# Optimization experiments

Measured on AMD Instinct MI355X. Metric: run time of the kernel, lower is better.

Reference implementation:

```python
import jax, jax.numpy as jnp
import numpy as np

B, T, D = 8, 2048, 1024   # batch, seq_len (== block_size), n_embed
HS = 128                   # head_size

def setup_inputs() -> dict:
    key = jax.random.key(0)
    kx, kk, kq, kv = jax.random.split(key, 4)
    s = D ** -0.5  # torch Linear default init scale ~ U(-1/sqrt(in), 1/sqrt(in))
    x  = jax.random.normal(kx, (B, T, D), dtype=jnp.float32)
    Wk = jax.random.uniform(kk, (HS, D), jnp.float32, -s, s)
    Wq = jax.random.uniform(kq, (HS, D), jnp.float32, -s, s)
    Wv = jax.random.uniform(kv, (HS, D), jnp.float32, -s, s)
    return {"x": x, "Wk": Wk, "Wq": Wq, "Wv": Wv}

def reference(x, Wk, Wq, Wv):
    # single-head causal self-attention; dropout disabled (eval mode)
    Tlen = x.shape[1]
    k = jnp.einsum('btd,hd->bth', x, Wk)   # [B,T,HS]
    q = jnp.einsum('btd,hd->bth', x, Wq)
    v = jnp.einsum('btd,hd->bth', x, Wv)
    scale = Wk.shape[0] ** -0.5
    scores = jnp.einsum('bth,bsh->bts', q, k) * scale   # [B,T,T]
    causal = jnp.tril(jnp.ones((Tlen, Tlen), dtype=bool))
    scores = jnp.where(causal, scores, -jnp.inf)
    weights = jax.nn.softmax(scores, axis=-1)
    out = jnp.einsum('bts,bsh->bth', weights, v)        # [B,T,HS]
    return out
```

## Files before the change

kernel.cpp:

```cpp
#include <hip/hip_runtime.h>
#include <hip/hip_bf16.h>
#include <math.h>

#define BATCH_N 8
#define SEQ_T   2048
#define DIM_D   1024
#define HS_N    128

using bf16x8_t = __attribute__((ext_vector_type(8))) __bf16;
using bf16x4_t = __attribute__((ext_vector_type(4))) __bf16;
using f32x4_t  = __attribute__((ext_vector_type(4))) float;

__device__ __forceinline__ f32x4_t mfma_16x16x32(bf16x8_t a, bf16x8_t b, f32x4_t c) {
  return __builtin_amdgcn_mfma_f32_16x16x32_bf16(a, b, c, 0, 0, 0);
}

__device__ __forceinline__ void async_cp16(const void* g, void* l) {
  __builtin_amdgcn_global_load_lds(
      (const __attribute__((address_space(1))) unsigned int*)g,
      (__attribute__((address_space(3))) unsigned int*)l, 16, 0, 0);
}

#define BAR()      __builtin_amdgcn_s_barrier()
#define FENCE()    asm volatile("" ::: "memory")
#define WAIT_VM(n) asm volatile("s_waitcnt vmcnt(" #n ")" ::: "memory")
#define WAIT_LGKM0 asm volatile("s_waitcnt lgkmcnt(0)" ::: "memory")

__global__ __launch_bounds__(256) void castw_kernel(
    const float* __restrict__ Wk, const float* __restrict__ Wq,
    const float* __restrict__ Wv, __bf16* __restrict__ Wb,
    unsigned int* __restrict__ km) {
  if (blockIdx.x == 0 && threadIdx.x < 8) km[threadIdx.x] = 0u;
  int idx = blockIdx.x * 256 + threadIdx.x;
  int e   = idx * 4;
  int row = e >> 10;
  int col = e & 1023;
  const float* src;
  float sc = 1.0f;
  if (row < 128) {
    src = Wk + row * DIM_D + col;
  } else if (row < 256) {
    src = Wq + (row - 128) * DIM_D + col;
    sc  = 0.08838834764831845f;
  } else {
    src = Wv + (row - 256) * DIM_D + col;
  }
  float4 v = *(const float4*)src;
  bf16x4_t o;
  o[0] = (__bf16)(v.x * sc); o[1] = (__bf16)(v.y * sc);
  o[2] = (__bf16)(v.z * sc); o[3] = (__bf16)(v.w * sc);
  *(bf16x4_t*)(Wb + e) = o;
}

__global__ __launch_bounds__(512, 2) void proj_kernel(
    const float* __restrict__ x, const __bf16* __restrict__ Wb,
    __bf16* __restrict__ Qb, __bf16* __restrict__ Kb, __bf16* __restrict__ Vt) {
  __shared__ __align__(16) char psmem[114688];
  __bf16* A = (__bf16*)psmem;

  const int tid  = threadIdx.x;
  const int lane = tid & 63;
  const int wave = tid >> 6;
  const int h    = wave >> 2;
  const int g    = wave & 3;
  const int lr = lane & 15;
  const int lq = lane >> 4;
  const int m0 = blockIdx.x * 64;

  f32x4_t acc[2][6];
  #pragma unroll
  for (int mt = 0; mt < 2; ++mt)
    #pragma unroll
    for (int nt = 0; nt < 6; ++nt) acc[mt][nt] = (f32x4_t){0.f, 0.f, 0.f, 0.f};

  auto stageB = [&](int bufi, int kt) {
    __bf16* Bs = (__bf16*)(psmem + 65536 + bufi * 24576);
    for (int c = wave; c < 24; c += 8) {
      const int row = c * 16 + (lane >> 2);
      const int u   = (lane & 3) ^ ((row >> 1) & 3);
      async_cp16(Wb + (size_t)row * DIM_D + kt * 32 + u * 8, Bs + c * 512);
    }
  };

  stageB(0, 0);

  for (int p = 0; p < 2; ++p) {
    __syncthreads();

    {
      const int r  = tid >> 3;
      const int t  = tid & 7;
      const float* xs = x + (size_t)(m0 + r) * DIM_D + p * 512;
      __bf16* as = A + r * 512;
      const int sw = r & 7;
      #pragma unroll
      for (int i = 0; i < 8; ++i) {
        const int u = t + 8 * i;
        float4 f0 = *(const float4*)(xs + u * 8);
        float4 f1 = *(const float4*)(xs + u * 8 + 4);
        bf16x8_t a;
        a[0] = (__bf16)f0.x; a[1] = (__bf16)f0.y;
        a[2] = (__bf16)f0.z; a[3] = (__bf16)f0.w;
        a[4] = (__bf16)f1.x; a[5] = (__bf16)f1.y;
        a[6] = (__bf16)f1.z; a[7] = (__bf16)f1.w;
        *(bf16x8_t*)(as + ((u ^ sw) * 8)) = a;
      }
    }
    __syncthreads();

    for (int kt2 = 0; kt2 < 16; ++kt2) {
      const int kt  = p * 16 + kt2;
      const int cur = kt & 1;
      if (kt + 1 < 32) {
        stageB(cur ^ 1, kt + 1);
        WAIT_VM(3);
      } else {
        WAIT_VM(0);
      }
      BAR();
      FENCE();
      const __bf16* Bs = (const __bf16*)(psmem + 65536 + cur * 24576);

      bf16x8_t af[2];
      #pragma unroll
      for (int mt = 0; mt < 2; ++mt) {
        const int ml = h * 32 + mt * 16 + lr;
        const int u  = kt2 * 4 + lq;
        af[mt] = *(const bf16x8_t*)(&A[ml * 512 + ((u ^ (ml & 7)) * 8)]);
      }
      bf16x8_t bfv[6];
      #pragma unroll
      for (int nt = 0; nt < 6; ++nt) {
        const int nl = g * 96 + nt * 16 + lr;
        bfv[nt] = *(const bf16x8_t*)(&Bs[nl * 32 + ((lq ^ ((nl >> 1) & 3)) * 8)]);
      }
      #pragma unroll
      for (int mt = 0; mt < 2; ++mt)
        #pragma unroll
        for (int nt = 0; nt < 6; ++nt)
          acc[mt][nt] = mfma_16x16x32(af[mt], bfv[nt], acc[mt][nt]);
      WAIT_LGKM0;
      BAR();
      FENCE();
    }
  }

  #pragma unroll
  for (int mt = 0; mt < 2; ++mt) {
    const int t0 = m0 + h * 32 + mt * 16 + lq * 4;
    #pragma unroll
    for (int nt = 0; nt < 6; ++nt) {
      const int nn = g * 96 + nt * 16 + lr;
      if (nn < 256) {
        __bf16* dst = (nn < 128) ? (Kb + nn) : (Qb + (nn - 128));
        #pragma unroll
        for (int r = 0; r < 4; ++r)
          dst[(size_t)(t0 + r) * HS_N] = (__bf16)acc[mt][nt][r];
      } else {
        const int bb = t0 >> 11;
        const int tl = t0 & 2047;
        bf16x4_t o;
        #pragma unroll
        for (int r = 0; r < 4; ++r) o[r] = (__bf16)acc[mt][nt][r];
        *(bf16x4_t*)(Vt + (size_t)bb * (HS_N * SEQ_T) + (size_t)(nn - 256) * SEQ_T + tl) = o;
      }
    }
  }
}

__global__ __launch_bounds__(256) void knorm_kernel(
    const __bf16* __restrict__ Kb, unsigned int* __restrict__ km) {
  const int t = blockIdx.x * 256 + threadIdx.x;
  const __bf16* kp = Kb + (size_t)t * HS_N;
  float ss = 0.f;
  #pragma unroll
  for (int i = 0; i < 16; ++i) {
    bf16x8_t v = *(const bf16x8_t*)(kp + i * 8);
    #pragma unroll
    for (int j = 0; j < 8; ++j) { float f = (float)v[j]; ss += f * f; }
  }
  #pragma unroll
  for (int off = 1; off < 64; off <<= 1) ss = fmaxf(ss, __shfl_xor(ss, off));
  if ((threadIdx.x & 63) == 0) atomicMax(km + (t >> 11), __float_as_uint(ss));
}

__global__ __launch_bounds__(256, 2) void attn_kernel(
    const __bf16* __restrict__ Qb, const __bf16* __restrict__ Kb,
    const __bf16* __restrict__ Vt, const unsigned int* __restrict__ km,
    __bf16* __restrict__ Opart, float* __restrict__ lpart) {
  __shared__ __align__(16) char smem[81920];
  __bf16* KsBase = (__bf16*)smem;
  __bf16* VsBase = (__bf16*)(smem + 32768);
  float*  Ofl    = (float*)smem;

  const int lane = threadIdx.x & 63;
  const int wave = threadIdx.x >> 6;
  const int lr = lane & 15;
  const int lq = lane >> 4;
  const int bid  = blockIdx.x;
  const int b    = bid & 7;
  const int rest = bid >> 3;
  const int jg   = 15 - (rest >> 2);
  const int p4   = rest & 3;
  const int Q0   = jg * 128;
  const int qa   = Q0 + wave * 32;
  const int ch   = 2 * (jg + 1);
  const int c0   = (p4 * ch) >> 2;
  const int c1   = ((p4 + 1) * ch) >> 2;

  const __bf16* Qbb = Qb + (size_t)b * (SEQ_T * HS_N);
  const __bf16* Kbb = Kb + (size_t)b * (SEQ_T * HS_N);
  const __bf16* Vbb = Vt + (size_t)b * (HS_N * SEQ_T);
  __bf16* pbA = (__bf16*)(smem + 65536 + wave * 4096);
  __bf16* pbB = (__bf16*)(smem + 65536 + wave * 4096 + 2048);

  bf16x8_t qf[2][4];
  #pragma unroll
  for (int t = 0; t < 2; ++t)
    #pragma unroll
    for (int ks = 0; ks < 4; ++ks)
      qf[t][ks] = *(const bf16x8_t*)(Qbb + (size_t)(qa + t * 16 + lr) * HS_N
                                     + ks * 32 + lq * 8);

  const float km2 = __uint_as_float(km[b]);
  float mrow[2][4];
  #pragma unroll
  for (int t = 0; t < 2; ++t) {
    float qn2 = 0.f;
    #pragma unroll
    for (int ks = 0; ks < 4; ++ks)
      #pragma unroll
      for (int j = 0; j < 8; ++j) { float f = (float)qf[t][ks][j]; qn2 += f * f; }
    qn2 += __shfl_xor(qn2, 16);
    qn2 += __shfl_xor(qn2, 32);
    #pragma unroll
    for (int r2 = 0; r2 < 4; ++r2)
      mrow[t][r2] = sqrtf(__shfl(qn2, lq * 4 + r2) * km2);
  }

  f32x4_t Oa[2][8];
  #pragma unroll
  for (int t = 0; t < 2; ++t)
    #pragma unroll
    for (int o = 0; o < 8; ++o) Oa[t][o] = (f32x4_t){0.f, 0.f, 0.f, 0.f};
  float lsum[2][4] = {{0.f,0.f,0.f,0.f},{0.f,0.f,0.f,0.f}};

  auto stage = [&](int bufi, int c) {
    const int kk = c * 64;
    __bf16* Ks = KsBase + bufi * 8192;
    for (int idx = wave; idx < 32; idx += 4) {
      if (idx < 16) {
        const int row = idx * 4 + (lane >> 4);
        const int u   = (lane & 15) ^ (row & 15);
        async_cp16(Kbb + (size_t)(kk + row) * HS_N + u * 8, Ks + idx * 512);
      } else {
        const int i2  = idx - 16;
        const int row = i2 * 8 + (lane >> 3);
        const int u   = (lane & 7) ^ (row & 7);
        async_cp16(Vbb + (size_t)row * SEQ_T + kk + u * 8, VsBase + bufi * 8192 + i2 * 512);
      }
    }
  };

  if (c0 < c1) stage(0, c0);
  __syncthreads();

  for (int c = c0; c < c1; ++c) {
    const int cur = (c - c0) & 1;
    if (c + 1 < c1) {
      stage(cur ^ 1, c + 1);
      WAIT_VM(8);
    } else {
      WAIT_VM(0);
    }
    BAR();
    FENCE();

    const int kk = c * 64;
    const __bf16* Ks = KsBase + cur * 8192;
    const __bf16* Vs = VsBase + cur * 8192;

    f32x4_t s0[4], s1[4];
    #pragma unroll
    for (int nt = 0; nt < 4; ++nt) {
      s0[nt] = (f32x4_t){0.f, 0.f, 0.f, 0.f};
      s1[nt] = (f32x4_t){0.f, 0.f, 0.f, 0.f};
    }
    #pragma unroll
    for (int ks = 0; ks < 4; ++ks)
      #pragma unroll
      for (int nt = 0; nt < 4; ++nt) {
        bf16x8_t kf = *(const bf16x8_t*)(
            &Ks[(nt * 16 + lr) * 128 + (((ks * 4 + lq) ^ lr) * 8)]);
        s0[nt] = mfma_16x16x32(qf[0][ks], kf, s0[nt]);
        s1[nt] = mfma_16x16x32(qf[1][ks], kf, s1[nt]);
      }
    const int q0a = qa, q0b = qa + 16;
    if (kk + 63 > q0a) {
      #pragma unroll
      for (int nt = 0; nt < 4; ++nt) {
        const int col = kk + nt * 16 + lr;
        #pragma unroll
        for (int r2 = 0; r2 < 4; ++r2)
          if (col > q0a + lq * 4 + r2) s0[nt][r2] = -INFINITY;
      }
    }
    if (kk + 63 > q0b) {
      #pragma unroll
      for (int nt = 0; nt < 4; ++nt) {
        const int col = kk + nt * 16 + lr;
        #pragma unroll
        for (int r2 = 0; r2 < 4; ++r2)
          if (col > q0b + lq * 4 + r2) s1[nt][r2] = -INFINITY;
      }
    }

    #pragma unroll
    for (int r2 = 0; r2 < 4; ++r2) {
      float a0 = __expf(s0[0][r2] - mrow[0][r2]);
      float a1 = __expf(s0[1][r2] - mrow[0][r2]);
      float a2 = __expf(s0[2][r2] - mrow[0][r2]);
      float a3 = __expf(s0[3][r2] - mrow[0][r2]);
      s0[0][r2] = a0; s0[1][r2] = a1; s0[2][r2] = a2; s0[3][r2] = a3;
      lsum[0][r2] += (a0 + a1) + (a2 + a3);
      float b0 = __expf(s1[0][r2] - mrow[1][r2]);
      float b1 = __expf(s1[1][r2] - mrow[1][r2]);
      float b2 = __expf(s1[2][r2] - mrow[1][r2]);
      float b3 = __expf(s1[3][r2] - mrow[1][r2]);
      s1[0][r2] = b0; s1[1][r2] = b1; s1[2][r2] = b2; s1[3][r2] = b3;
      lsum[1][r2] += (b0 + b1) + (b2 + b3);
    }

    #pragma unroll
    for (int nt = 0; nt < 4; ++nt)
      #pragma unroll
      for (int r2 = 0; r2 < 4; ++r2) {
        const int prow = lq * 4 + r2;
        const int pcol = (nt * 16 + lr) ^ ((prow & 7) << 3);
        pbA[prow * 64 + pcol] = (__bf16)s0[nt][r2];
        pbB[prow * 64 + pcol] = (__bf16)s1[nt][r2];
      }

    #pragma unroll
    for (int k2 = 0; k2 < 2; ++k2) {
      const int au = ((k2 * 4 + lq) ^ (lr & 7)) << 3;
      bf16x8_t afrA = *(const bf16x8_t*)(pbA + lr * 64 + au);
      bf16x8_t afrB = *(const bf16x8_t*)(pbB + lr * 64 + au);
      #pragma unroll
      for (int o = 0; o < 8; ++o) {
        bf16x8_t vfr = *(const bf16x8_t*)(
            &Vs[(o * 16 + lr) * 64 + (((k2 * 4 + lq) ^ (lr & 7)) * 8)]);
        Oa[0][o] = mfma_16x16x32(afrA, vfr, Oa[0][o]);
        Oa[1][o] = mfma_16x16x32(afrB, vfr, Oa[1][o]);
      }
    }
    WAIT_LGKM0;
    BAR();
    FENCE();
  }

  #pragma unroll
  for (int t = 0; t < 2; ++t)
    #pragma unroll
    for (int r2 = 0; r2 < 4; ++r2) {
      float v = lsum[t][r2];
      v += __shfl_xor(v, 1);
      v += __shfl_xor(v, 2);
      v += __shfl_xor(v, 4);
      v += __shfl_xor(v, 8);
      if (lr == 0)
        lpart[bid * 128 + wave * 32 + t * 16 + lq * 4 + r2] = v;
    }

  #pragma unroll
  for (int t = 0; t < 2; ++t)
    #pragma unroll
    for (int o = 0; o < 8; ++o)
      #pragma unroll
      for (int r2 = 0; r2 < 4; ++r2)
        Ofl[(wave * 32 + t * 16 + lq * 4 + r2) * 132 + o * 16 + lr] = Oa[t][o][r2];
  __syncthreads();

  {
    const int row = threadIdx.x >> 1;
    const int cb  = (threadIdx.x & 1) * 64;
    __bf16* dst = Opart + ((size_t)bid * 128 + row) * 128 + cb;
    #pragma unroll
    for (int g2 = 0; g2 < 16; ++g2) {
      float4 f = *(const float4*)(&Ofl[row * 132 + cb + g2 * 4]);
      bf16x4_t o;
      o[0] = (__bf16)f.x; o[1] = (__bf16)f.y; o[2] = (__bf16)f.z; o[3] = (__bf16)f.w;
      *(bf16x4_t*)(dst + g2 * 4) = o;
    }
  }
}

__global__ __launch_bounds__(256) void merge_kernel(
    const __bf16* __restrict__ Opart, const float* __restrict__ lpart,
    float* __restrict__ out) {
  const int idx = blockIdx.x * 256 + threadIdx.x;
  const int row = idx >> 5;
  const int c4  = (idx & 31) * 4;
  const int b   = row >> 11;
  const int tl  = row & 2047;
  const int jg  = tl >> 7;
  const int lrow = tl & 127;
  const int rbase = (15 - jg) * 4;
  float a0 = 0.f, a1 = 0.f, a2 = 0.f, a3 = 0.f, l = 0.f;
  #pragma unroll
  for (int p = 0; p < 4; ++p) {
    const int s = b + 8 * (rbase + p);
    bf16x4_t a = *(const bf16x4_t*)(Opart + ((size_t)s * 128 + lrow) * 128 + c4);
    a0 += (float)a[0]; a1 += (float)a[1]; a2 += (float)a[2]; a3 += (float)a[3];
    l += lpart[s * 128 + lrow];
  }
  const float inv = 1.0f / l;
  float4 o;
  o.x = a0 * inv; o.y = a1 * inv; o.z = a2 * inv; o.w = a3 * inv;
  *(float4*)(out + (size_t)row * HS_N + c4) = o;
}

extern "C" void kernel_launch(void* const* d_in, const int* in_sizes, int n_in,
                              void* d_out, int out_size, void* d_ws, size_t ws_size,
                              hipStream_t stream) {
  const float* x  = (const float*)d_in[0];
  const float* Wk = (const float*)d_in[1];
  const float* Wq = (const float*)d_in[2];
  const float* Wv = (const float*)d_in[3];
  float* out = (float*)d_out;

  char* ws = (char*)d_ws;
  __bf16* Wb = (__bf16*)ws;
  __bf16* Qb = (__bf16*)(ws + 786432);
  __bf16* Kb = (__bf16*)(ws + 786432 + 4194304);
  __bf16* Vt = (__bf16*)(ws + 786432 + 8388608);
  unsigned int* km = (unsigned int*)(ws + 13369344);
  __bf16* Opart = (__bf16*)(ws + 13369600);
  float*  lpart = (float*)(ws + 30146816);

  castw_kernel<<<384, 256, 0, stream>>>(Wk, Wq, Wv, Wb, km);
  proj_kernel<<<256, 512, 0, stream>>>(x, Wb, Qb, Kb, Vt);
  knorm_kernel<<<64, 256, 0, stream>>>(Kb, km);
  attn_kernel<<<512, 256, 0, stream>>>(Qb, Kb, Vt, km, Opart, lpart);
  merge_kernel<<<2048, 256, 0, stream>>>(Opart, lpart, out);
}
```

Measured before the change: 156.6 us.

## Fuse key-norm max into projection epilogue and triple-buffer weight tiles

Removes the separate knorm kernel and computes per-row squared norms of K inside the projection epilogue from fp32 accumulators, reducing via LDS atomics and a global atomicMax. It also turns the weight staging from double to triple buffering with deeper vmcnt waits, raising LDS to 136KB and lowering launch bounds to one block per CU. This saves a launch and a reread of K, but trades occupancy for deeper prefetch. Norms now come from fp32 values rather than rounded bf16, which only slightly changes the bound.

```diff
diff --git a/kernel.cpp b/kernel.cpp
--- a/kernel.cpp
+++ b/kernel.cpp
@@ -52,10 +52,11 @@
   *(bf16x4_t*)(Wb + e) = o;
 }
 
-__global__ __launch_bounds__(512, 2) void proj_kernel(
+__global__ __launch_bounds__(512, 1) void proj_kernel(
     const float* __restrict__ x, const __bf16* __restrict__ Wb,
-    __bf16* __restrict__ Qb, __bf16* __restrict__ Kb, __bf16* __restrict__ Vt) {
-  __shared__ __align__(16) char psmem[114688];
+    __bf16* __restrict__ Qb, __bf16* __restrict__ Kb, __bf16* __restrict__ Vt,
+    unsigned int* __restrict__ km) {
+  __shared__ __align__(16) char psmem[139264];
   __bf16* A = (__bf16*)psmem;
 
   const int tid  = threadIdx.x;
@@ -73,8 +74,8 @@
     #pragma unroll
     for (int nt = 0; nt < 6; ++nt) acc[mt][nt] = (f32x4_t){0.f, 0.f, 0.f, 0.f};
 
-  auto stageB = [&](int bufi, int kt) {
-    __bf16* Bs = (__bf16*)(psmem + 65536 + bufi * 24576);
+  auto stageB = [&](int kt) {
+    __bf16* Bs = (__bf16*)(psmem + 65536 + (kt % 3) * 24576);
     for (int c = wave; c < 24; c += 8) {
       const int row = c * 16 + (lane >> 2);
       const int u   = (lane & 3) ^ ((row >> 1) & 3);
@@ -82,7 +83,8 @@
     }
   };
 
-  stageB(0, 0);
+  stageB(0);
+  stageB(1);
 
   for (int p = 0; p < 2; ++p) {
     __syncthreads();
@@ -109,17 +111,14 @@
     __syncthreads();
 
     for (int kt2 = 0; kt2 < 16; ++kt2) {
-      const int kt  = p * 16 + kt2;
-      const int cur = kt & 1;
-      if (kt + 1 < 32) {
-        stageB(cur ^ 1, kt + 1);
-        WAIT_VM(3);
-      } else {
-        WAIT_VM(0);
-      }
+      const int kt = p * 16 + kt2;
+      if (kt + 2 < 32) stageB(kt + 2);
+      if (kt < 30)       { WAIT_VM(6); }
+      else if (kt == 30) { WAIT_VM(3); }
+      else               { WAIT_VM(0); }
       BAR();
       FENCE();
-      const __bf16* Bs = (const __bf16*)(psmem + 65536 + cur * 24576);
+      const __bf16* Bs = (const __bf16*)(psmem + 65536 + (kt % 3) * 24576);
 
       bf16x8_t af[2];
       #pragma unroll
@@ -143,6 +142,32 @@
       BAR();
       FENCE();
     }
+  }
+
+  __syncthreads();
+  float* rowss = (float*)psmem;
+  if (tid < 64) rowss[tid] = 0.f;
+  __syncthreads();
+  if (g < 2) {
+    #pragma unroll
+    for (int mt = 0; mt < 2; ++mt)
+      #pragma unroll
+      for (int r = 0; r < 4; ++r) {
+        float s = 0.f;
+        #pragma unroll
+        for (int nt = 0; nt < 6; ++nt)
+          if (g == 0 || nt < 2) s += acc[mt][nt][r] * acc[mt][nt][r];
+        s += __shfl_xor(s, 1); s += __shfl_xor(s, 2);
+        s += __shfl_xor(s, 4); s += __shfl_xor(s, 8);
+        if (lr == 0) atomicAdd(&rowss[h * 32 + mt * 16 + lq * 4 + r], s);
+      }
+  }
+  __syncthreads();
+  if (tid < 64) {
+    float v = rowss[tid];
+    #pragma unroll
+    for (int off = 1; off < 64; off <<= 1) v = fmaxf(v, __shfl_xor(v, off));
+    if (tid == 0) atomicMax(km + (m0 >> 11), __float_as_uint(v));
   }
 
   #pragma unroll
@@ -166,22 +191,6 @@
       }
     }
   }
-}
-
-__global__ __launch_bounds__(256) void knorm_kernel(
-    const __bf16* __restrict__ Kb, unsigned int* __restrict__ km) {
-  const int t = blockIdx.x * 256 + threadIdx.x;
-  const __bf16* kp = Kb + (size_t)t * HS_N;
-  float ss = 0.f;
-  #pragma unroll
-  for (int i = 0; i < 16; ++i) {
-    bf16x8_t v = *(const bf16x8_t*)(kp + i * 8);
-    #pragma unroll
-    for (int j = 0; j < 8; ++j) { float f = (float)v[j]; ss += f * f; }
-  }
-  #pragma unroll
-  for (int off = 1; off < 64; off <<= 1) ss = fmaxf(ss, __shfl_xor(ss, off));
-  if ((threadIdx.x & 63) == 0) atomicMax(km + (t >> 11), __float_as_uint(ss));
 }
 
 __global__ __launch_bounds__(256, 2) void attn_kernel(
@@ -439,8 +448,7 @@
   float*  lpart = (float*)(ws + 30146816);
 
   castw_kernel<<<384, 256, 0, stream>>>(Wk, Wq, Wv, Wb, km);
-  proj_kernel<<<256, 512, 0, stream>>>(x, Wb, Qb, Kb, Vt);
-  knorm_kernel<<<64, 256, 0, stream>>>(Kb, km);
+  proj_kernel<<<256, 512, 0, stream>>>(x, Wb, Qb, Kb, Vt, km);
   attn_kernel<<<512, 256, 0, stream>>>(Qb, Kb, Vt, km, Opart, lpart);
   merge_kernel<<<2048, 256, 0, stream>>>(Opart, lpart, out);
 }
```

Result: faster. 151.3 us (-3.4%).
